# Optimization experiments

Measured on AMD Instinct MI355X. Metric: run time of the kernel, lower is better.

Reference implementation:

```python
import jax, jax.numpy as jnp
import numpy as np

S, B, IN, H, DFF, OUT, L, NHEAD, WINDOW = 2048, 4, 64, 1024, 1024, 64, 3, 4, 4
EPS = 1e-5


def _layer_norm(x, scale, bias):
    m = jnp.mean(x, axis=-1, keepdims=True)
    v = jnp.var(x, axis=-1, keepdims=True)
    return (x - m) * jax.lax.rsqrt(v + EPS) * scale + bias


def setup_inputs() -> dict:
    key = jax.random.key(0)
    ks = jax.random.split(key, 12)
    s = 0.02
    return {
        "src": jax.random.normal(ks[0], (S, B, IN), dtype=jnp.float32),
        "Wenc": jax.random.normal(ks[1], (H, IN), dtype=jnp.float32) * s,
        "benc": jnp.zeros((H,), jnp.float32),
        "Wqkv": jax.random.normal(ks[2], (L, 3 * H, H), dtype=jnp.float32) * s,
        "bqkv": jnp.zeros((L, 3 * H), jnp.float32),
        "Wo": jax.random.normal(ks[3], (L, H, H), dtype=jnp.float32) * s,
        "bo": jnp.zeros((L, H), jnp.float32),
        "W1": jax.random.normal(ks[4], (L, DFF, H), dtype=jnp.float32) * s,
        "b1": jnp.zeros((L, DFF), jnp.float32),
        "W2": jax.random.normal(ks[5], (L, H, DFF), dtype=jnp.float32) * s,
        "b2": jnp.zeros((L, H), jnp.float32),
        "ln1_s": jnp.ones((L, H), jnp.float32),
        "ln1_b": jnp.zeros((L, H), jnp.float32),
        "ln2_s": jnp.ones((L, H), jnp.float32),
        "ln2_b": jnp.zeros((L, H), jnp.float32),
        "Wout": jax.random.normal(ks[6], (OUT, H), dtype=jnp.float32) * s,
        "bout": jnp.zeros((OUT,), jnp.float32),
    }


def _banded_mask(sz):
    # triu(1) masked + lower-band (j < i-4) masked => allowed: i-4 <= j <= i
    i = jnp.arange(sz)[:, None]
    j = jnp.arange(sz)[None, :]
    allowed = (j <= i) & (j >= i - WINDOW)
    return jnp.where(allowed, 0.0, -1e9).astype(jnp.float32)


def reference(src, Wenc, benc, Wqkv, bqkv, Wo, bo, W1, b1, W2, b2,
              ln1_s, ln1_b, ln2_s, ln2_b, Wout, bout):
    dh = H // NHEAD
    mask = _banded_mask(src.shape[0])  # [S, S]
    x = src @ Wenc.T + benc  # [S, B, H]  (NOTE: pos_encoder is never applied in the source)

    def layer(x, p):
        Wqkv_, bqkv_, Wo_, bo_, W1_, b1_, W2_, b2_, s1, g1, s2, g2 = p
        qkv = x @ Wqkv_.T + bqkv_  # [S, B, 3H]
        q, k, v = jnp.split(qkv, 3, axis=-1)
        sS, sB = x.shape[0], x.shape[1]
        q = q.reshape(sS, sB, NHEAD, dh)
        k = k.reshape(sS, sB, NHEAD, dh)
        v = v.reshape(sS, sB, NHEAD, dh)
        scores = jnp.einsum('sbhd,tbhd->bhst', q, k) / jnp.sqrt(jnp.float32(dh))
        scores = scores + mask  # broadcast over [b, h]
        attn = jax.nn.softmax(scores, axis=-1)
        ctx = jnp.einsum('bhst,tbhd->sbhd', attn, v).reshape(sS, sB, H)
        attn_out = ctx @ Wo_.T + bo_
        x = _layer_norm(x + attn_out, s1, g1)  # post-norm (PyTorch default)
        ff = jax.nn.relu(x @ W1_.T + b1_) @ W2_.T + b2_
        x = _layer_norm(x + ff, s2, g2)
        return x, None

    x, _ = jax.lax.scan(layer, x, (Wqkv, bqkv, Wo, bo, W1, b1, W2, b2,
                                   ln1_s, ln1_b, ln2_s, ln2_b))
    return x @ Wout.T + bout  # [S, B, OUT]
```

## Files before the change

kernel.cpp:

```cpp
#include <hip/hip_runtime.h>
#include <hip/hip_bf16.h>

#define S_LEN   2048
#define BATCH   4
#define IN_DIM  64
#define H_DIM   1024
#define DFF_DIM 1024
#define OUT_DIM 64
#define NLAYER  3
#define NHEADS  4
#define DHEAD   256
#define WIN     4
#define ROWS    (S_LEN*BATCH)
#define QKV_LD  (3*H_DIM)


typedef __bf16 bf16x8 __attribute__((ext_vector_type(8)));
typedef float  f32x4  __attribute__((ext_vector_type(4)));

__device__ __forceinline__ float bfbits2f(unsigned int u) {
  union { unsigned int i; float f; } c; c.i = u << 16; return c.f;
}
__device__ __forceinline__ unsigned short f2bfbits(float f) {
  __hip_bfloat16 h = __float2bfloat16(f);
  return __builtin_bit_cast(unsigned short, h);
}

__device__ __forceinline__ void g2l16(const void* g, void* l) {
  __builtin_amdgcn_global_load_lds((__attribute__((address_space(1))) void*)g,
                                   (__attribute__((address_space(3))) void*)l,
                                   16, 0, 0);
}

__global__ __launch_bounds__(256)
void cvt_k(const float* __restrict__ in, __hip_bfloat16* __restrict__ out, int n)
{
  int i = (blockIdx.x * 256 + threadIdx.x) * 4;
  if (i >= n) return;
  float4 v = *(const float4*)(in + i);
  uint2 o;
  o.x = (unsigned)f2bfbits(v.x) | ((unsigned)f2bfbits(v.y) << 16);
  o.y = (unsigned)f2bfbits(v.z) | ((unsigned)f2bfbits(v.w) << 16);
  *(uint2*)(out + i) = o;
}

template<int RELU, int OUTF32, int ADDRES>
__global__ __launch_bounds__(256, 2)
void gemm_bt(const __hip_bfloat16* __restrict__ A, int lda,
             const __hip_bfloat16* __restrict__ B,
             const float* __restrict__ bias,
             void* __restrict__ Cp, int ldc,
             const __hip_bfloat16* __restrict__ R, int ldr,
             int M, int N, int K)
{
  __shared__ __align__(16) __hip_bfloat16 As[128 * 64];
  __shared__ __align__(16) __hip_bfloat16 Bs[128 * 64];

  const int tid  = threadIdx.x;
  const int lane = tid & 63;
  const int wave = tid >> 6;
  const int quad = lane >> 4;
  const int l16  = lane & 15;
  const int m0 = blockIdx.y * 128;
  const int n0 = blockIdx.x * 128;
  const int wr = (wave >> 1) * 64;
  const int wc = (wave & 1) * 64;

  int arow[4], acol[4], brow[4];
#pragma unroll
  for (int s = 0; s < 4; s++) {
    const int p = tid + (s << 8);
    arow[s] = p >> 3;
    acol[s] = ((p & 7) ^ ((p >> 3) & 7)) * 8;
    brow[s] = min(n0 + arow[s], N - 1);
  }

  f32x4 acc[4][4] = {};
  const int nk = K >> 6;

  for (int t = 0; t < nk; ++t) {
    const int k0 = t << 6;
#pragma unroll
    for (int s = 0; s < 4; s++) {
      const int lo = (wave * 64 + (s << 8)) * 8;
      g2l16(A + (size_t)(m0 + arow[s]) * lda + k0 + acol[s], &As[lo]);
      g2l16(B + (size_t)brow[s] * K + k0 + acol[s], &Bs[lo]);
    }
    __syncthreads();

#pragma unroll
    for (int kh = 0; kh < 2; kh++) {
      bf16x8 af[4], bfr[4];
#pragma unroll
      for (int i = 0; i < 4; i++) {
        const int row = wr + i * 16 + l16;
        const int c   = (kh * 4 + quad) ^ (row & 7);
        af[i] = *(const bf16x8*)&As[row * 64 + c * 8];
      }
#pragma unroll
      for (int j = 0; j < 4; j++) {
        const int row = wc + j * 16 + l16;
        const int c   = (kh * 4 + quad) ^ (row & 7);
        bfr[j] = *(const bf16x8*)&Bs[row * 64 + c * 8];
      }
#pragma unroll
      for (int i = 0; i < 4; i++)
#pragma unroll
        for (int j = 0; j < 4; j++)
          acc[i][j] = __builtin_amdgcn_mfma_f32_16x16x32_bf16(af[i], bfr[j], acc[i][j], 0, 0, 0);
    }
    __syncthreads();
  }

#pragma unroll
  for (int j = 0; j < 4; j++) {
    int col = n0 + wc + j * 16 + l16;
    if (col < N) {
      float bv = bias[col];
#pragma unroll
      for (int i = 0; i < 4; i++) {
        int row = m0 + wr + i * 16 + quad * 4;
#pragma unroll
        for (int r = 0; r < 4; r++) {
          float v = acc[i][j][r] + bv;
          if (RELU) v = fmaxf(v, 0.f);
          if (ADDRES) v += __bfloat162float(R[(size_t)(row + r) * ldr + col]);
          if (OUTF32) ((float*)Cp)[(size_t)(row + r) * ldc + col] = v;
          else ((__hip_bfloat16*)Cp)[(size_t)(row + r) * ldc + col] = __float2bfloat16(v);
        }
      }
    }
  }
}

__global__ __launch_bounds__(256)
void attn_k(__hip_bfloat16* __restrict__ qkv)
{
  const int gw   = (blockIdx.x << 2) + (threadIdx.x >> 6);
  const int lane = threadIdx.x & 63;
  const int h = gw & (NHEADS - 1);
  const int b = (gw >> 2) & (BATCH - 1);
  const int s = gw >> 4;
  const size_t hoff = (size_t)h * DHEAD + (lane << 2);

  float q0, q1, q2, q3;
  {
    uint2 t = *(const uint2*)(qkv + (size_t)(s * BATCH + b) * QKV_LD + hoff);
    q0 = bfbits2f(t.x & 0xffff); q1 = bfbits2f(t.x >> 16);
    q2 = bfbits2f(t.y & 0xffff); q3 = bfbits2f(t.y >> 16);
  }

  float sc[WIN + 1];
#pragma unroll
  for (int jj = 0; jj <= WIN; jj++) {
    int j = s - WIN + jj;
    float v = -1e30f;
    if (j >= 0) {
      uint2 t = *(const uint2*)(qkv + (size_t)(j * BATCH + b) * QKV_LD + H_DIM + hoff);
      float p = q0 * bfbits2f(t.x & 0xffff) + q1 * bfbits2f(t.x >> 16)
              + q2 * bfbits2f(t.y & 0xffff) + q3 * bfbits2f(t.y >> 16);
#pragma unroll
      for (int o = 32; o; o >>= 1) p += __shfl_xor(p, o);
      v = p * 0.0625f;
    }
    sc[jj] = v;
  }

  float mx = sc[0];
#pragma unroll
  for (int jj = 1; jj <= WIN; jj++) mx = fmaxf(mx, sc[jj]);
  float p[WIN + 1], den = 0.f;
#pragma unroll
  for (int jj = 0; jj <= WIN; jj++) { p[jj] = __expf(sc[jj] - mx); den += p[jj]; }

  float a0 = 0.f, a1 = 0.f, a2 = 0.f, a3 = 0.f;
#pragma unroll
  for (int jj = 0; jj <= WIN; jj++) {
    int j = s - WIN + jj;
    if (j >= 0) {
      uint2 t = *(const uint2*)(qkv + (size_t)(j * BATCH + b) * QKV_LD + 2 * H_DIM + hoff);
      a0 += p[jj] * bfbits2f(t.x & 0xffff); a1 += p[jj] * bfbits2f(t.x >> 16);
      a2 += p[jj] * bfbits2f(t.y & 0xffff); a3 += p[jj] * bfbits2f(t.y >> 16);
    }
  }
  float rl = 1.f / den;
  uint2 o;
  o.x = (unsigned)f2bfbits(a0 * rl) | ((unsigned)f2bfbits(a1 * rl) << 16);
  o.y = (unsigned)f2bfbits(a2 * rl) | ((unsigned)f2bfbits(a3 * rl) << 16);
  *(uint2*)(qkv + (size_t)(s * BATCH + b) * QKV_LD + hoff) = o;
}

__global__ __launch_bounds__(256)
void ln_k(const __hip_bfloat16* __restrict__ y, int ys,
          const float* __restrict__ g, const float* __restrict__ be,
          __hip_bfloat16* __restrict__ xout)
{
  const int row = blockIdx.x, tid = threadIdx.x;
  uint2 yv = *(const uint2*)(y + (size_t)row * ys + tid * 4);
  float t0 = bfbits2f(yv.x & 0xffff);
  float t1 = bfbits2f(yv.x >> 16);
  float t2 = bfbits2f(yv.y & 0xffff);
  float t3 = bfbits2f(yv.y >> 16);
  float s  = t0 + t1 + t2 + t3;
  float ss = t0 * t0 + t1 * t1 + t2 * t2 + t3 * t3;
#pragma unroll
  for (int o = 32; o; o >>= 1) { s += __shfl_down(s, o); ss += __shfl_down(ss, o); }
  __shared__ float rs[4], rss[4];
  if ((tid & 63) == 0) { rs[tid >> 6] = s; rss[tid >> 6] = ss; }
  __syncthreads();
  float S  = rs[0] + rs[1] + rs[2] + rs[3];
  float SS = rss[0] + rss[1] + rss[2] + rss[3];
  const float inv = 1.f / (float)H_DIM;
  float mean = S * inv;
  float var  = SS * inv - mean * mean;
  float rstd = rsqrtf(var + 1e-5f);
  float4 gv = *(const float4*)(g + tid * 4);
  float4 bv = *(const float4*)(be + tid * 4);
  float o0 = (t0 - mean) * rstd * gv.x + bv.x;
  float o1 = (t1 - mean) * rstd * gv.y + bv.y;
  float o2 = (t2 - mean) * rstd * gv.z + bv.z;
  float o3 = (t3 - mean) * rstd * gv.w + bv.w;
  uint2 ob;
  ob.x = (unsigned)f2bfbits(o0) | ((unsigned)f2bfbits(o1) << 16);
  ob.y = (unsigned)f2bfbits(o2) | ((unsigned)f2bfbits(o3) << 16);
  *(uint2*)(xout + (size_t)row * H_DIM + tid * 4) = ob;
}

extern "C" void kernel_launch(void* const* d_in, const int* in_sizes, int n_in,
                              void* d_out, int out_size, void* d_ws, size_t ws_size,
                              hipStream_t stream) {
  const float* src   = (const float*)d_in[0];
  const float* Wenc  = (const float*)d_in[1];
  const float* benc  = (const float*)d_in[2];
  const float* Wqkv  = (const float*)d_in[3];
  const float* bqkv  = (const float*)d_in[4];
  const float* Wo    = (const float*)d_in[5];
  const float* bo    = (const float*)d_in[6];
  const float* W1    = (const float*)d_in[7];
  const float* b1    = (const float*)d_in[8];
  const float* W2    = (const float*)d_in[9];
  const float* b2    = (const float*)d_in[10];
  const float* ln1s  = (const float*)d_in[11];
  const float* ln1b  = (const float*)d_in[12];
  const float* ln2s  = (const float*)d_in[13];
  const float* ln2b  = (const float*)d_in[14];
  const float* Wout  = (const float*)d_in[15];
  const float* bout  = (const float*)d_in[16];

  char* ws = (char*)d_ws;
  __hip_bfloat16* WB   = (__hip_bfloat16*)ws;
  __hip_bfloat16* srcb = WB;
  __hip_bfloat16* wenc = WB + 524288;
  __hip_bfloat16* wqkv = WB + 589824;
  __hip_bfloat16* wo   = WB + 10027008;
  __hip_bfloat16* w1   = WB + 13172736;
  __hip_bfloat16* w2   = WB + 16318464;
  __hip_bfloat16* wout = WB + 19464192;
  __hip_bfloat16* xb  = (__hip_bfloat16*)(ws + (size_t)40 * 1048576);
  __hip_bfloat16* qkv = (__hip_bfloat16*)(ws + (size_t)56 * 1048576);
  __hip_bfloat16* ctxp = qkv;
  __hip_bfloat16* ybuf = qkv + H_DIM;
  __hip_bfloat16* hbuf = qkv + 2 * H_DIM;

  const dim3 blk(256);
  #define CVT(inp, outp, n) cvt_k<<<dim3(((n) / 4 + 255) / 256), blk, 0, stream>>>(inp, outp, n)

  CVT(src,  srcb, 524288);
  CVT(Wenc, wenc, 65536);
  CVT(Wqkv, wqkv, 9437184);
  CVT(Wo,   wo,   3145728);
  CVT(W1,   w1,   3145728);
  CVT(W2,   w2,   3145728);
  CVT(Wout, wout, 65536);

  gemm_bt<0, 0, 0><<<dim3(H_DIM / 128, ROWS / 128), blk, 0, stream>>>(
      srcb, IN_DIM, wenc, benc, xb, H_DIM, nullptr, 0, ROWS, H_DIM, IN_DIM);

  for (int l = 0; l < NLAYER; l++) {
    gemm_bt<0, 0, 0><<<dim3(QKV_LD / 128, ROWS / 128), blk, 0, stream>>>(
        xb, H_DIM, wqkv + (size_t)l * QKV_LD * H_DIM, bqkv + l * QKV_LD,
        qkv, QKV_LD, nullptr, 0, ROWS, QKV_LD, H_DIM);
    attn_k<<<dim3(ROWS * NHEADS / 4), blk, 0, stream>>>(qkv);
    gemm_bt<0, 0, 1><<<dim3(H_DIM / 128, ROWS / 128), blk, 0, stream>>>(
        ctxp, QKV_LD, wo + (size_t)l * H_DIM * H_DIM, bo + l * H_DIM,
        ybuf, QKV_LD, xb, H_DIM, ROWS, H_DIM, H_DIM);
    ln_k<<<dim3(ROWS), blk, 0, stream>>>(ybuf, QKV_LD, ln1s + l * H_DIM, ln1b + l * H_DIM, xb);
    gemm_bt<1, 0, 0><<<dim3(DFF_DIM / 128, ROWS / 128), blk, 0, stream>>>(
        xb, H_DIM, w1 + (size_t)l * DFF_DIM * H_DIM, b1 + l * DFF_DIM,
        hbuf, QKV_LD, nullptr, 0, ROWS, DFF_DIM, H_DIM);
    gemm_bt<0, 0, 1><<<dim3(H_DIM / 128, ROWS / 128), blk, 0, stream>>>(
        hbuf, QKV_LD, w2 + (size_t)l * H_DIM * DFF_DIM, b2 + l * H_DIM,
        ybuf, QKV_LD, xb, H_DIM, ROWS, H_DIM, DFF_DIM);
    ln_k<<<dim3(ROWS), blk, 0, stream>>>(ybuf, QKV_LD, ln2s + l * H_DIM, ln2b + l * H_DIM, xb);
  }

  gemm_bt<0, 1, 0><<<dim3(1, ROWS / 128), blk, 0, stream>>>(
      xb, H_DIM, wout, bout, d_out, OUT_DIM, nullptr, 0, ROWS, OUT_DIM, H_DIM);
}
```

Baseline: 737.5 us.

## Merge weight conversions, swizzle GEMM tile order, use one wave per LayerNorm row

The seven fp32-to-bf16 conversion launches become one kernel that walks a list of segments, cutting launch overhead. GEMM blocks are remapped so groups of four M-tiles share N-tiles, aiming for better L2 reuse of weight tiles. LayerNorm now gives each row to one 64-lane wave with 16 elements per lane and a shuffle-only reduction, removing the shared-memory barrier and quartering the block count. The GEMM remap relies on the M-tile count dividing by four, which holds for these grid shapes.

```diff
diff --git a/kernel.cpp b/kernel.cpp
--- a/kernel.cpp
+++ b/kernel.cpp
@@ -32,16 +32,27 @@
                                    16, 0, 0);
 }
 
+struct CvtSeg { const float* src; __hip_bfloat16* dst; int n4; };
+
 __global__ __launch_bounds__(256)
-void cvt_k(const float* __restrict__ in, __hip_bfloat16* __restrict__ out, int n)
+void cvt_all_k(CvtSeg s0, CvtSeg s1, CvtSeg s2, CvtSeg s3,
+               CvtSeg s4, CvtSeg s5, CvtSeg s6)
 {
-  int i = (blockIdx.x * 256 + threadIdx.x) * 4;
-  if (i >= n) return;
-  float4 v = *(const float4*)(in + i);
+  int i = blockIdx.x * 256 + threadIdx.x;
+  CvtSeg seg;
+  if      (i < s0.n4) { seg = s0; }
+  else if ((i -= s0.n4) < s1.n4) { seg = s1; }
+  else if ((i -= s1.n4) < s2.n4) { seg = s2; }
+  else if ((i -= s2.n4) < s3.n4) { seg = s3; }
+  else if ((i -= s3.n4) < s4.n4) { seg = s4; }
+  else if ((i -= s4.n4) < s5.n4) { seg = s5; }
+  else if ((i -= s5.n4) < s6.n4) { seg = s6; }
+  else return;
+  float4 v = *(const float4*)(seg.src + (size_t)i * 4);
   uint2 o;
   o.x = (unsigned)f2bfbits(v.x) | ((unsigned)f2bfbits(v.y) << 16);
   o.y = (unsigned)f2bfbits(v.z) | ((unsigned)f2bfbits(v.w) << 16);
-  *(uint2*)(out + i) = o;
+  *(uint2*)(seg.dst + (size_t)i * 4) = o;
 }
 
 template<int RELU, int OUTF32, int ADDRES>
@@ -61,8 +72,15 @@
   const int wave = tid >> 6;
   const int quad = lane >> 4;
   const int l16  = lane & 15;
-  const int m0 = blockIdx.y * 128;
-  const int n0 = blockIdx.x * 128;
+
+  const int gx  = gridDim.x;
+  const int lin = blockIdx.y * gx + blockIdx.x;
+  const int gsz = 4 * gx;
+  const int mt  = (lin / gsz) * 4 + (lin & 3);
+  const int nt  = (lin % gsz) >> 2;
+  const int m0 = mt * 128;
+  const int n0 = nt * 128;
+
   const int wr = (wave >> 1) * 64;
   const int wc = (wave & 1) * 64;
 
@@ -195,35 +213,52 @@
           const float* __restrict__ g, const float* __restrict__ be,
           __hip_bfloat16* __restrict__ xout)
 {
-  const int row = blockIdx.x, tid = threadIdx.x;
-  uint2 yv = *(const uint2*)(y + (size_t)row * ys + tid * 4);
-  float t0 = bfbits2f(yv.x & 0xffff);
-  float t1 = bfbits2f(yv.x >> 16);
-  float t2 = bfbits2f(yv.y & 0xffff);
-  float t3 = bfbits2f(yv.y >> 16);
-  float s  = t0 + t1 + t2 + t3;
-  float ss = t0 * t0 + t1 * t1 + t2 * t2 + t3 * t3;
-#pragma unroll
-  for (int o = 32; o; o >>= 1) { s += __shfl_down(s, o); ss += __shfl_down(ss, o); }
-  __shared__ float rs[4], rss[4];
-  if ((tid & 63) == 0) { rs[tid >> 6] = s; rss[tid >> 6] = ss; }
-  __syncthreads();
-  float S  = rs[0] + rs[1] + rs[2] + rs[3];
-  float SS = rss[0] + rss[1] + rss[2] + rss[3];
-  const float inv = 1.f / (float)H_DIM;
-  float mean = S * inv;
-  float var  = SS * inv - mean * mean;
-  float rstd = rsqrtf(var + 1e-5f);
-  float4 gv = *(const float4*)(g + tid * 4);
-  float4 bv = *(const float4*)(be + tid * 4);
-  float o0 = (t0 - mean) * rstd * gv.x + bv.x;
-  float o1 = (t1 - mean) * rstd * gv.y + bv.y;
-  float o2 = (t2 - mean) * rstd * gv.z + bv.z;
-  float o3 = (t3 - mean) * rstd * gv.w + bv.w;
-  uint2 ob;
-  ob.x = (unsigned)f2bfbits(o0) | ((unsigned)f2bfbits(o1) << 16);
-  ob.y = (unsigned)f2bfbits(o2) | ((unsigned)f2bfbits(o3) << 16);
-  *(uint2*)(xout + (size_t)row * H_DIM + tid * 4) = ob;
+  const int row  = blockIdx.x * 4 + (threadIdx.x >> 6);
+  const int lane = threadIdx.x & 63;
+  const int e0   = lane * 16;
+  const __hip_bfloat16* yp = y + (size_t)row * ys + e0;
+
+  uint2 v[4];
+  *(uint4*)&v[0] = *(const uint4*)yp;
+  *(uint4*)&v[2] = *(const uint4*)(yp + 8);
+  float t[16];
+#pragma unroll
+  for (int k = 0; k < 4; k++) {
+    t[k * 4 + 0] = bfbits2f(v[k].x & 0xffff);
+    t[k * 4 + 1] = bfbits2f(v[k].x >> 16);
+    t[k * 4 + 2] = bfbits2f(v[k].y & 0xffff);
+    t[k * 4 + 3] = bfbits2f(v[k].y >> 16);
+  }
+  float s = 0.f, ss = 0.f;
+#pragma unroll
+  for (int k = 0; k < 16; k++) { s += t[k]; ss += t[k] * t[k]; }
+#pragma unroll
+  for (int o = 32; o; o >>= 1) { s += __shfl_xor(s, o); ss += __shfl_xor(ss, o); }
+
+  const float inv  = 1.f / (float)H_DIM;
+  const float mean = s * inv;
+  const float var  = ss * inv - mean * mean;
+  const float rstd = rsqrtf(var + 1e-5f);
+
+  float4 gv[4], bv[4];
+#pragma unroll
+  for (int k = 0; k < 4; k++) {
+    gv[k] = *(const float4*)(g + e0 + k * 4);
+    bv[k] = *(const float4*)(be + e0 + k * 4);
+  }
+  uint2 ob[4];
+#pragma unroll
+  for (int k = 0; k < 4; k++) {
+    float o0 = (t[k*4+0] - mean) * rstd * gv[k].x + bv[k].x;
+    float o1 = (t[k*4+1] - mean) * rstd * gv[k].y + bv[k].y;
+    float o2 = (t[k*4+2] - mean) * rstd * gv[k].z + bv[k].z;
+    float o3 = (t[k*4+3] - mean) * rstd * gv[k].w + bv[k].w;
+    ob[k].x = (unsigned)f2bfbits(o0) | ((unsigned)f2bfbits(o1) << 16);
+    ob[k].y = (unsigned)f2bfbits(o2) | ((unsigned)f2bfbits(o3) << 16);
+  }
+  __hip_bfloat16* xp = xout + (size_t)row * H_DIM + e0;
+  *(uint4*)xp       = *(const uint4*)&ob[0];
+  *(uint4*)(xp + 8) = *(const uint4*)&ob[2];
 }
 
 extern "C" void kernel_launch(void* const* d_in, const int* in_sizes, int n_in,
@@ -263,15 +298,18 @@
   __hip_bfloat16* hbuf = qkv + 2 * H_DIM;
 
   const dim3 blk(256);
-  #define CVT(inp, outp, n) cvt_k<<<dim3(((n) / 4 + 255) / 256), blk, 0, stream>>>(inp, outp, n)
-
-  CVT(src,  srcb, 524288);
-  CVT(Wenc, wenc, 65536);
-  CVT(Wqkv, wqkv, 9437184);
-  CVT(Wo,   wo,   3145728);
-  CVT(W1,   w1,   3145728);
-  CVT(W2,   w2,   3145728);
-  CVT(Wout, wout, 65536);
+
+  {
+    CvtSeg s0{src,  srcb, 524288 / 4};
+    CvtSeg s1{Wenc, wenc, 65536 / 4};
+    CvtSeg s2{Wqkv, wqkv, 9437184 / 4};
+    CvtSeg s3{Wo,   wo,   3145728 / 4};
+    CvtSeg s4{W1,   w1,   3145728 / 4};
+    CvtSeg s5{W2,   w2,   3145728 / 4};
+    CvtSeg s6{Wout, wout, 65536 / 4};
+    const int tot4 = (524288 + 65536 + 9437184 + 3 * 3145728 + 65536) / 4;
+    cvt_all_k<<<dim3((tot4 + 255) / 256), blk, 0, stream>>>(s0, s1, s2, s3, s4, s5, s6);
+  }
 
   gemm_bt<0, 0, 0><<<dim3(H_DIM / 128, ROWS / 128), blk, 0, stream>>>(
       srcb, IN_DIM, wenc, benc, xb, H_DIM, nullptr, 0, ROWS, H_DIM, IN_DIM);
@@ -284,14 +322,14 @@
     gemm_bt<0, 0, 1><<<dim3(H_DIM / 128, ROWS / 128), blk, 0, stream>>>(
         ctxp, QKV_LD, wo + (size_t)l * H_DIM * H_DIM, bo + l * H_DIM,
         ybuf, QKV_LD, xb, H_DIM, ROWS, H_DIM, H_DIM);
-    ln_k<<<dim3(ROWS), blk, 0, stream>>>(ybuf, QKV_LD, ln1s + l * H_DIM, ln1b + l * H_DIM, xb);
+    ln_k<<<dim3(ROWS / 4), blk, 0, stream>>>(ybuf, QKV_LD, ln1s + l * H_DIM, ln1b + l * H_DIM, xb);
     gemm_bt<1, 0, 0><<<dim3(DFF_DIM / 128, ROWS / 128), blk, 0, stream>>>(
         xb, H_DIM, w1 + (size_t)l * DFF_DIM * H_DIM, b1 + l * DFF_DIM,
         hbuf, QKV_LD, nullptr, 0, ROWS, DFF_DIM, H_DIM);
     gemm_bt<0, 0, 1><<<dim3(H_DIM / 128, ROWS / 128), blk, 0, stream>>>(
         hbuf, QKV_LD, w2 + (size_t)l * H_DIM * DFF_DIM, b2 + l * H_DIM,
         ybuf, QKV_LD, xb, H_DIM, ROWS, H_DIM, DFF_DIM);
-    ln_k<<<dim3(ROWS), blk, 0, stream>>>(ybuf, QKV_LD, ln2s + l * H_DIM, ln2b + l * H_DIM, xb);
+    ln_k<<<dim3(ROWS / 4), blk, 0, stream>>>(ybuf, QKV_LD, ln2s + l * H_DIM, ln2b + l * H_DIM, xb);
   }
 
   gemm_bt<0, 1, 0><<<dim3(1, ROWS / 128), blk, 0, stream>>>(
```

After: 728.5 us. About the same (-1.2%).
